# Optimization experiments

Measured on AMD Instinct MI355X. Metric: run time of the kernel, lower is better.

Reference implementation:

```python
import jax, jax.numpy as jnp
import numpy as np

N = 8192
IN_F = 256
HEADS = 4
HF = 64            # head_features = out_features / heads
OUT_F = HEADS * HF # concat=True
NEG_SLOPE = 0.2


def setup_inputs() -> dict:
    key = jax.random.key(0)
    ks = jax.random.split(key, 7)
    x = jax.random.normal(ks[0], (N, IN_F), dtype=jnp.float32)
    graph = jax.random.randint(ks[1], (N, N), 0, 2, dtype=jnp.int32)
    weight = jax.random.normal(ks[2], (HEADS, IN_F, HF), dtype=jnp.float32) * (1.0 / np.sqrt(IN_F))
    weight_i = jax.random.normal(ks[3], (HEADS, HF, 1), dtype=jnp.float32) * (1.0 / np.sqrt(HF))
    weight_j = jax.random.normal(ks[4], (HEADS, HF, 1), dtype=jnp.float32) * (1.0 / np.sqrt(HF))
    weight_r = jax.random.normal(ks[5], (IN_F, HF * HEADS), dtype=jnp.float32) * (1.0 / np.sqrt(IN_F))
    bias = jnp.zeros((OUT_F,), dtype=jnp.float32)
    return {"x": x, "graph": graph, "weight": weight, "weight_i": weight_i,
            "weight_j": weight_j, "weight_r": weight_r, "bias": bias}


def reference(x, graph, weight, weight_i, weight_j, weight_r, bias):
    # h: per-head projected features [heads, N, hf]
    h = jnp.einsum('nm,hmf->hnf', x, weight)
    # additive attention logits: coe_i [h,N,1] + coe_j [h,1,N]
    coe_i = jnp.einsum('hnf,hfo->hno', h, weight_i)          # [heads, N, 1]
    coe_j = jnp.einsum('hnf,hfo->hno', h, weight_j)          # [heads, N, 1]
    coe = jax.nn.leaky_relu(coe_i + jnp.swapaxes(coe_j, 1, 2), NEG_SLOPE)  # [heads, N, N]
    # adjacency mask (note transpose, matching the torch code)
    mask = jnp.where(graph > 0, 0.0, -jnp.inf).T             # [N, N]
    att = jax.nn.softmax(coe + mask[None], axis=-1)          # [heads, N, N]
    # aggregate and move heads to axis 1: [N, heads, hf]
    y = jnp.einsum('hij,hjf->ihf', att, h)
    # residual with projection (in_features != head_features)
    y = y + (x @ weight_r).reshape(N, HEADS, HF)
    # concat heads + bias
    y = y.reshape(N, OUT_F) + bias
    return y
```

## Files before the change

### kernel.cpp

```cpp
#include <hip/hip_runtime.h>
#include <hip/hip_bf16.h>

#define N 8192
#define IN_F 256
#define HEADS 4
#define HF 64
#define OUT_F 256

typedef __attribute__((ext_vector_type(8))) short short8;
typedef __attribute__((ext_vector_type(4))) float f32x4;

__device__ __forceinline__ float lrelu(float x) {
    return fmaxf(x, 0.0f) * 0.8f + x * 0.2f;
}
__device__ __forceinline__ short f2bf(float f) {
    union { __hip_bfloat16 h; short s; } u;
    u.h = __float2bfloat16(f);
    return u.s;
}
__device__ __forceinline__ float bf2f(unsigned short b) {
    union { unsigned u; float f; } v; v.u = ((unsigned)b) << 16;
    return v.f;
}

__global__ __launch_bounds__(256) void k_wcvt(
    const float* __restrict__ w, const float* __restrict__ wr,
    unsigned short* __restrict__ BbT)
{
    int c = blockIdx.x;
    int k = threadIdx.x;
    float v;
    if (c < 256) {
        int head = c >> 6, f = c & 63;
        v = w[((size_t)head * IN_F + k) * HF + f];
    } else {
        v = wr[(size_t)k * OUT_F + (c - 256)];
    }
    BbT[(size_t)c * IN_F + k] = (unsigned short)f2bf(v);
}

__global__ __launch_bounds__(256) void k_gemm(
    const float* __restrict__ x, const unsigned short* __restrict__ BbT,
    const float* __restrict__ bias,
    unsigned short* __restrict__ h, float* __restrict__ out)
{
    __shared__ unsigned short Asw[64 * 64];
    __shared__ unsigned short Bsw[128 * 64];
    int t = threadIdx.x;
    int m0 = blockIdx.x * 64;
    int bn = blockIdx.y;
    int w_ = t >> 6, l = t & 63;
    int wr_ = w_ >> 1, wc_ = w_ & 1;
    int ar = l & 15, g = l >> 4;

    f32x4 acc[2][4];
    #pragma unroll
    for (int m = 0; m < 2; ++m)
        #pragma unroll
        for (int n = 0; n < 4; ++n) acc[m][n] = (f32x4){0.f, 0.f, 0.f, 0.f};

    int srow = t >> 2, skq = (t & 3) * 16;
    int sc = t >> 1, sh = (t & 1) * 32;

    for (int kt = 0; kt < 4; ++kt) {
        const float* xs = x + (size_t)(m0 + srow) * IN_F + kt * 64 + skq;
        float4 xa = ((const float4*)xs)[0];
        float4 xb = ((const float4*)xs)[1];
        float4 xc = ((const float4*)xs)[2];
        float4 xd = ((const float4*)xs)[3];
        unsigned short ae[16];
        ae[0] = f2bf(xa.x); ae[1] = f2bf(xa.y); ae[2] = f2bf(xa.z); ae[3] = f2bf(xa.w);
        ae[4] = f2bf(xb.x); ae[5] = f2bf(xb.y); ae[6] = f2bf(xb.z); ae[7] = f2bf(xb.w);
        ae[8] = f2bf(xc.x); ae[9] = f2bf(xc.y); ae[10] = f2bf(xc.z); ae[11] = f2bf(xc.w);
        ae[12] = f2bf(xd.x); ae[13] = f2bf(xd.y); ae[14] = f2bf(xd.z); ae[15] = f2bf(xd.w);
        int kb0 = (skq >> 3) ^ (srow & 7);
        int kb1 = ((skq >> 3) + 1) ^ (srow & 7);
        *(uint4*)&Asw[srow * 64 + kb0 * 8] = *(uint4*)&ae[0];
        *(uint4*)&Asw[srow * 64 + kb1 * 8] = *(uint4*)&ae[8];
        const unsigned short* bs = BbT + (size_t)(bn * 128 + sc) * IN_F + kt * 64 + sh;
        uint4 b0 = ((const uint4*)bs)[0];
        uint4 b1 = ((const uint4*)bs)[1];
        uint4 b2 = ((const uint4*)bs)[2];
        uint4 b3 = ((const uint4*)bs)[3];
        int hb = sh >> 3;
        *(uint4*)&Bsw[sc * 64 + ((hb + 0) ^ (sc & 7)) * 8] = b0;
        *(uint4*)&Bsw[sc * 64 + ((hb + 1) ^ (sc & 7)) * 8] = b1;
        *(uint4*)&Bsw[sc * 64 + ((hb + 2) ^ (sc & 7)) * 8] = b2;
        *(uint4*)&Bsw[sc * 64 + ((hb + 3) ^ (sc & 7)) * 8] = b3;
        __syncthreads();
        #pragma unroll
        for (int ks = 0; ks < 2; ++ks) {
            short8 af[2], bf[4];
            #pragma unroll
            for (int m = 0; m < 2; ++m) {
                int row = wr_ * 32 + m * 16 + ar;
                int kb = (ks * 4 + g) ^ (row & 7);
                af[m] = *(const short8*)&Asw[row * 64 + kb * 8];
            }
            #pragma unroll
            for (int n = 0; n < 4; ++n) {
                int c = wc_ * 64 + n * 16 + ar;
                int kb = (ks * 4 + g) ^ (c & 7);
                bf[n] = *(const short8*)&Bsw[c * 64 + kb * 8];
            }
            #pragma unroll
            for (int m = 0; m < 2; ++m)
                #pragma unroll
                for (int n = 0; n < 4; ++n)
                    acc[m][n] = __builtin_amdgcn_mfma_f32_16x16x32_bf16(af[m], bf[n], acc[m][n], 0, 0, 0);
        }
        __syncthreads();
    }
    #pragma unroll
    for (int m = 0; m < 2; ++m) {
        #pragma unroll
        for (int n = 0; n < 4; ++n) {
            int cg = bn * 128 + wc_ * 64 + n * 16 + ar;
            #pragma unroll
            for (int r = 0; r < 4; ++r) {
                int mg = m0 + wr_ * 32 + m * 16 + g * 4 + r;
                float v = acc[m][n][r];
                if (cg < 256) {
                    int head = cg >> 6, f = cg & 63;
                    h[((size_t)head * N + mg) * HF + f] = (unsigned short)f2bf(v);
                } else {
                    out[(size_t)mg * OUT_F + (cg - 256)] = v + bias[cg - 256];
                }
            }
        }
    }
}

__global__ __launch_bounds__(256) void k_tr(
    const unsigned short* __restrict__ h, const float* __restrict__ wi,
    const float* __restrict__ wj,
    unsigned short* __restrict__ hT, float* __restrict__ coe_i, float* __restrict__ coe_j)
{
    __shared__ unsigned short tl[64 * 66];
    __shared__ float red_i[4][64];
    __shared__ float red_j[4][64];
    int t = threadIdx.x;
    int head = blockIdx.y;
    int n0 = blockIdx.x * 64;
    int nr = t >> 2, c0 = (t & 3) * 16;
    const unsigned short* src = h + ((size_t)(head * N + n0 + nr) * HF) + c0;
    uint4 v0 = *(const uint4*)src;
    uint4 v1 = *(const uint4*)(src + 8);
    unsigned short e[16];
    *(uint4*)&e[0] = v0;
    *(uint4*)&e[8] = v1;
    #pragma unroll
    for (int k = 0; k < 16; ++k)
        tl[(c0 + k) * 66 + nr] = e[k];
    __syncthreads();
    int f = t >> 2, nc = (t & 3) * 16;
    unsigned int ov[8];
    #pragma unroll
    for (int k = 0; k < 8; ++k)
        ov[k] = *(const unsigned int*)&tl[f * 66 + nc + 2 * k];
    unsigned short* dst = hT + ((size_t)(head * HF + f) * N) + n0 + nc;
    uint4 o0, o1;
    o0.x = ov[0]; o0.y = ov[1]; o0.z = ov[2]; o0.w = ov[3];
    o1.x = ov[4]; o1.y = ov[5]; o1.z = ov[6]; o1.w = ov[7];
    *(uint4*)dst = o0;
    *(uint4*)(dst + 8) = o1;
    int q = t >> 6, nn = t & 63;
    float pi = 0.f, pj = 0.f;
    #pragma unroll
    for (int k = 0; k < 16; ++k) {
        int ff = q * 16 + k;
        float hv = bf2f(tl[ff * 66 + nn]);
        pi = fmaf(hv, wi[head * HF + ff], pi);
        pj = fmaf(hv, wj[head * HF + ff], pj);
    }
    red_i[q][nn] = pi;
    red_j[q][nn] = pj;
    __syncthreads();
    if (t < 64) {
        float si = red_i[0][t] + red_i[1][t] + red_i[2][t] + red_i[3][t];
        float sj = red_j[0][t] + red_j[1][t] + red_j[2][t] + red_j[3][t];
        coe_i[head * N + n0 + t] = si;
        coe_j[head * N + n0 + t] = sj;
    }
}

__global__ __launch_bounds__(256) void k_cols(
    const float* __restrict__ coe_j, float* __restrict__ maxB,
    float* __restrict__ F, float* __restrict__ H)
{
    __shared__ float red[256];
    int head = blockIdx.x;
    int t = threadIdx.x;
    float m = -1e30f;
    for (int n = t; n < N; n += 256) {
        float b = coe_j[head * N + n];
        F[head * N + n] = __expf(b);
        H[head * N + n] = __expf(0.2f * b);
        m = fmaxf(m, b);
    }
    red[t] = m;
    __syncthreads();
    for (int s = 128; s > 0; s >>= 1) {
        if (t < s) red[t] = fmaxf(red[t], red[t + s]);
        __syncthreads();
    }
    if (t == 0) maxB[head] = red[0];
}

__global__ __launch_bounds__(256) void k_pack(
    const int* __restrict__ graph, unsigned int* __restrict__ bits)
{
    int i = blockIdx.y * 256 + threadIdx.x;
    int jw = blockIdx.x;
    const int* gp = graph + (size_t)(jw * 32) * N + i;
    unsigned int word = 0;
    #pragma unroll
    for (int k = 0; k < 32; ++k)
        word |= (gp[(size_t)k * N] > 0 ? 1u : 0u) << k;
    bits[(size_t)jw * N + i] = word;
}

__device__ __forceinline__ void computeP(short8& af,
    const float4& fa, const float4& fb, const float4& ha, const float4& hb,
    unsigned int mk, float Ei, float Gi)
{
    float fv[8] = {fa.x, fa.y, fa.z, fa.w, fb.x, fb.y, fb.z, fb.w};
    float hv[8] = {ha.x, ha.y, ha.z, ha.w, hb.x, hb.y, hb.z, hb.w};
    #pragma unroll
    for (int j = 0; j < 8; ++j) {
        float p = fmaxf(Ei * fv[j], Gi * hv[j]);
        p = (mk & (1u << j)) ? p : 0.0f;
        af[j] = f2bf(p);
    }
}

__global__ __launch_bounds__(512) void k_att(
    const unsigned short* __restrict__ hT, const float* __restrict__ coe_i,
    const float* __restrict__ maxB, const float* __restrict__ F,
    const float* __restrict__ H, const unsigned int* __restrict__ bits,
    float* __restrict__ out)
{
    __shared__ unsigned short hbuf[2][64 * 64];
    __shared__ float mbuf[4 * 64 * 21];

    int t = threadIdx.x;
    int head = blockIdx.x;
    int i0 = blockIdx.y * 64;
    int w = t >> 6;
    int l = t & 63;
    int wrow = w & 3;
    int grp = w >> 2;
    int ar = l & 15, g = l >> 4, g8 = g * 8;

    int irow = i0 + wrow * 16 + ar;
    float a = coe_i[head * N + irow];
    float M = lrelu(a + maxB[head]);
    float Ei = __expf(a - M);
    float Gi = __expf(0.2f * a - M);

    f32x4 acc[4];
    #pragma unroll
    for (int fb = 0; fb < 4; ++fb) acc[fb] = (f32x4){0.f, 0.f, 0.f, 0.f};
    f32x4 accd = (f32x4){0.f, 0.f, 0.f, 0.f};

    short8 ones;
    #pragma unroll
    for (int k = 0; k < 8; ++k) ones[k] = (short)0x3F80;

    int sbuf = t >> 8;
    int u = t & 255;
    int sf = u >> 2;
    int sj = (u & 3) * 16;
    const unsigned short* hrow = hT + ((size_t)(head * HF + sf) * N) + sj;
    int pg0 = ((sj >> 3) + 0) ^ (sf & 7);
    int pg1 = ((sj >> 3) + 1) ^ (sf & 7);
    unsigned short* wp0 = &hbuf[sbuf][sf * 64 + pg0 * 8];
    unsigned short* wp1 = &hbuf[sbuf][sf * 64 + pg1 * 8];

    const float* Fp = F + head * N + g8;
    const float* Hp = H + head * N + g8;
    const unsigned int* bp = bits + irow;

    for (int jt0 = 0; jt0 < N; jt0 += 128) {
        int jt = jt0 + grp * 64;
        uint4 hv0 = *(const uint4*)(hrow + jt0 + sbuf * 64);
        uint4 hv1 = *(const uint4*)(hrow + jt0 + sbuf * 64 + 8);
        unsigned int mk0 = bp[(size_t)((jt >> 5) + 0) * N] >> g8;
        unsigned int mk1 = bp[(size_t)((jt >> 5) + 1) * N] >> g8;
        float4 f0 = *(const float4*)(Fp + jt);
        float4 f1 = *(const float4*)(Fp + jt + 4);
        float4 f2 = *(const float4*)(Fp + jt + 32);
        float4 f3 = *(const float4*)(Fp + jt + 36);
        float4 h0 = *(const float4*)(Hp + jt);
        float4 h1 = *(const float4*)(Hp + jt + 4);
        float4 h2 = *(const float4*)(Hp + jt + 32);
        float4 h3 = *(const float4*)(Hp + jt + 36);

        __syncthreads();
        *(uint4*)wp0 = hv0;
        *(uint4*)wp1 = hv1;
        __syncthreads();

        short8 af0, af1;
        computeP(af0, f0, f1, h0, h1, mk0, Ei, Gi);
        computeP(af1, f2, f3, h2, h3, mk1, Ei, Gi);

        #pragma unroll
        for (int ss = 0; ss < 2; ++ss) {
            short8 af = ss ? af1 : af0;
            #pragma unroll
            for (int fb = 0; fb < 4; ++fb) {
                int row = fb * 16 + ar;
                int pg = (ss * 4 + g) ^ (ar & 7);
                short8 bfr = *(const short8*)&hbuf[grp][row * 64 + pg * 8];
                acc[fb] = __builtin_amdgcn_mfma_f32_16x16x32_bf16(af, bfr, acc[fb], 0, 0, 0);
            }
            accd = __builtin_amdgcn_mfma_f32_16x16x32_bf16(af, ones, accd, 0, 0, 0);
        }
    }

    __syncthreads();
    int mb = (wrow * 64 + l) * 21;
    if (grp == 1) {
        #pragma unroll
        for (int fb = 0; fb < 4; ++fb)
            #pragma unroll
            for (int r = 0; r < 4; ++r)
                mbuf[mb + fb * 4 + r] = acc[fb][r];
        #pragma unroll
        for (int r = 0; r < 4; ++r)
            mbuf[mb + 16 + r] = accd[r];
    }
    __syncthreads();
    if (grp == 0) {
        #pragma unroll
        for (int fb = 0; fb < 4; ++fb)
            #pragma unroll
            for (int r = 0; r < 4; ++r)
                acc[fb][r] += mbuf[mb + fb * 4 + r];
        #pragma unroll
        for (int r = 0; r < 4; ++r)
            accd[r] += mbuf[mb + 16 + r];
        #pragma unroll
        for (int r = 0; r < 4; ++r) {
            float inv = 1.0f / accd[r];
            int orow = i0 + wrow * 16 + g * 4 + r;
            float* op = out + (size_t)orow * OUT_F + head * HF + ar;
            #pragma unroll
            for (int fb = 0; fb < 4; ++fb)
                op[fb * 16] += acc[fb][r] * inv;
        }
    }
}

extern "C" void kernel_launch(void* const* d_in, const int* in_sizes, int n_in,
                              void* d_out, int out_size, void* d_ws, size_t ws_size,
                              hipStream_t stream) {
    const float* x     = (const float*)d_in[0];
    const int*   graph = (const int*)d_in[1];
    const float* w     = (const float*)d_in[2];
    const float* wi    = (const float*)d_in[3];
    const float* wj    = (const float*)d_in[4];
    const float* wr    = (const float*)d_in[5];
    const float* bias  = (const float*)d_in[6];
    float* out = (float*)d_out;

    char* ws = (char*)d_ws;
    unsigned short* h   = (unsigned short*)(ws);
    unsigned short* hT  = (unsigned short*)(ws + (4u << 20));
    float* coe_i = (float*)(ws + (8u << 20));
    float* coe_j = (float*)(ws + (8u << 20) + 131072);
    float* maxB  = (float*)(ws + (8u << 20) + 2 * 131072);
    float* F     = (float*)(ws + (8u << 20) + 2 * 131072 + 1024);
    float* H     = (float*)(ws + (8u << 20) + 3 * 131072 + 1024);
    unsigned short* BbT = (unsigned short*)(ws + (8u << 20) + 4 * 131072 + 1024);
    unsigned int* bits  = (unsigned int*)(ws + (8u << 20) + 4 * 131072 + 1024 + 262144);

    k_wcvt<<<dim3(512), 256, 0, stream>>>(w, wr, BbT);
    k_gemm<<<dim3(128, 4), 256, 0, stream>>>(x, BbT, bias, h, out);
    k_tr<<<dim3(128, 4), 256, 0, stream>>>(h, wi, wj, hT, coe_i, coe_j);
    k_cols<<<dim3(4), 256, 0, stream>>>(coe_j, maxB, F, H);
    k_pack<<<dim3(256, 32), 256, 0, stream>>>(graph, bits);
    k_att<<<dim3(HEADS, N / 64), 512, 0, stream>>>(hT, coe_i, maxB, F, H, bits, out);
}
```

Measured before the change: 180.9 us.

## Write transposed h from GEMM, register-prefetch attention tiles, pack bf16 conversions

The GEMM epilogue now writes h directly in transposed layout, so the separate transpose kernel is removed and replaced by a simple coefficient kernel that reads hT. The attention kernel prefetches the next hT tile into registers and double-buffers shared memory, which drops one barrier per iteration. It also aliases the merge buffer onto the same shared memory, swaps the grid axes, adds a launch-bounds occupancy hint, and builds P with packed bf16 conversion and branchless masking. The aim is to cut an intermediate round trip through memory and reduce barrier stalls in the main loop, at the cost of more register pressure and strided 8-byte stores from the GEMM.

```diff
diff --git a/kernel.cpp b/kernel.cpp
--- a/kernel.cpp
+++ b/kernel.cpp
@@ -21,6 +21,11 @@
 __device__ __forceinline__ float bf2f(unsigned short b) {
     union { unsigned u; float f; } v; v.u = ((unsigned)b) << 16;
     return v.f;
+}
+__device__ __forceinline__ unsigned pack_bf16(float p0, float p1) {
+    union { __hip_bfloat162 b; unsigned u; } cv;
+    cv.b = __float22bfloat162_rn(make_float2(p0, p1));
+    return cv.u;
 }
 
 __global__ __launch_bounds__(256) void k_wcvt(
@@ -42,7 +47,7 @@
 __global__ __launch_bounds__(256) void k_gemm(
     const float* __restrict__ x, const unsigned short* __restrict__ BbT,
     const float* __restrict__ bias,
-    unsigned short* __restrict__ h, float* __restrict__ out)
+    unsigned short* __restrict__ hT, float* __restrict__ out)
 {
     __shared__ unsigned short Asw[64 * 64];
     __shared__ unsigned short Bsw[128 * 64];
@@ -68,15 +73,15 @@
         float4 xb = ((const float4*)xs)[1];
         float4 xc = ((const float4*)xs)[2];
         float4 xd = ((const float4*)xs)[3];
-        unsigned short ae[16];
-        ae[0] = f2bf(xa.x); ae[1] = f2bf(xa.y); ae[2] = f2bf(xa.z); ae[3] = f2bf(xa.w);
-        ae[4] = f2bf(xb.x); ae[5] = f2bf(xb.y); ae[6] = f2bf(xb.z); ae[7] = f2bf(xb.w);
-        ae[8] = f2bf(xc.x); ae[9] = f2bf(xc.y); ae[10] = f2bf(xc.z); ae[11] = f2bf(xc.w);
-        ae[12] = f2bf(xd.x); ae[13] = f2bf(xd.y); ae[14] = f2bf(xd.z); ae[15] = f2bf(xd.w);
+        unsigned ae[8];
+        ae[0] = pack_bf16(xa.x, xa.y); ae[1] = pack_bf16(xa.z, xa.w);
+        ae[2] = pack_bf16(xb.x, xb.y); ae[3] = pack_bf16(xb.z, xb.w);
+        ae[4] = pack_bf16(xc.x, xc.y); ae[5] = pack_bf16(xc.z, xc.w);
+        ae[6] = pack_bf16(xd.x, xd.y); ae[7] = pack_bf16(xd.z, xd.w);
         int kb0 = (skq >> 3) ^ (srow & 7);
         int kb1 = ((skq >> 3) + 1) ^ (srow & 7);
         *(uint4*)&Asw[srow * 64 + kb0 * 8] = *(uint4*)&ae[0];
-        *(uint4*)&Asw[srow * 64 + kb1 * 8] = *(uint4*)&ae[8];
+        *(uint4*)&Asw[srow * 64 + kb1 * 8] = *(uint4*)&ae[4];
         const unsigned short* bs = BbT + (size_t)(bn * 128 + sc) * IN_F + kt * 64 + sh;
         uint4 b0 = ((const uint4*)bs)[0];
         uint4 b1 = ((const uint4*)bs)[1];
@@ -116,72 +121,39 @@
         #pragma unroll
         for (int n = 0; n < 4; ++n) {
             int cg = bn * 128 + wc_ * 64 + n * 16 + ar;
-            #pragma unroll
-            for (int r = 0; r < 4; ++r) {
-                int mg = m0 + wr_ * 32 + m * 16 + g * 4 + r;
-                float v = acc[m][n][r];
-                if (cg < 256) {
-                    int head = cg >> 6, f = cg & 63;
-                    h[((size_t)head * N + mg) * HF + f] = (unsigned short)f2bf(v);
-                } else {
-                    out[(size_t)mg * OUT_F + (cg - 256)] = v + bias[cg - 256];
-                }
+            int mg0 = m0 + wr_ * 32 + m * 16 + g * 4;
+            if (cg < 256) {
+                int head = cg >> 6, f = cg & 63;
+                unsigned pk[2];
+                pk[0] = pack_bf16(acc[m][n][0], acc[m][n][1]);
+                pk[1] = pack_bf16(acc[m][n][2], acc[m][n][3]);
+                *(uint2*)(hT + (size_t)(head * HF + f) * N + mg0) = *(uint2*)pk;
+            } else {
+                float bb = bias[cg - 256];
+                #pragma unroll
+                for (int r = 0; r < 4; ++r)
+                    out[(size_t)(mg0 + r) * OUT_F + (cg - 256)] = acc[m][n][r] + bb;
             }
         }
     }
 }
 
-__global__ __launch_bounds__(256) void k_tr(
-    const unsigned short* __restrict__ h, const float* __restrict__ wi,
-    const float* __restrict__ wj,
-    unsigned short* __restrict__ hT, float* __restrict__ coe_i, float* __restrict__ coe_j)
-{
-    __shared__ unsigned short tl[64 * 66];
-    __shared__ float red_i[4][64];
-    __shared__ float red_j[4][64];
-    int t = threadIdx.x;
+__global__ __launch_bounds__(256) void k_coe(
+    const unsigned short* __restrict__ hT, const float* __restrict__ wi,
+    const float* __restrict__ wj, float* __restrict__ coe_i, float* __restrict__ coe_j)
+{
     int head = blockIdx.y;
-    int n0 = blockIdx.x * 64;
-    int nr = t >> 2, c0 = (t & 3) * 16;
-    const unsigned short* src = h + ((size_t)(head * N + n0 + nr) * HF) + c0;
-    uint4 v0 = *(const uint4*)src;
-    uint4 v1 = *(const uint4*)(src + 8);
-    unsigned short e[16];
-    *(uint4*)&e[0] = v0;
-    *(uint4*)&e[8] = v1;
-    #pragma unroll
-    for (int k = 0; k < 16; ++k)
-        tl[(c0 + k) * 66 + nr] = e[k];
-    __syncthreads();
-    int f = t >> 2, nc = (t & 3) * 16;
-    unsigned int ov[8];
-    #pragma unroll
-    for (int k = 0; k < 8; ++k)
-        ov[k] = *(const unsigned int*)&tl[f * 66 + nc + 2 * k];
-    unsigned short* dst = hT + ((size_t)(head * HF + f) * N) + n0 + nc;
-    uint4 o0, o1;
-    o0.x = ov[0]; o0.y = ov[1]; o0.z = ov[2]; o0.w = ov[3];
-    o1.x = ov[4]; o1.y = ov[5]; o1.z = ov[6]; o1.w = ov[7];
-    *(uint4*)dst = o0;
-    *(uint4*)(dst + 8) = o1;
-    int q = t >> 6, nn = t & 63;
-    float pi = 0.f, pj = 0.f;
-    #pragma unroll
-    for (int k = 0; k < 16; ++k) {
-        int ff = q * 16 + k;
-        float hv = bf2f(tl[ff * 66 + nn]);
-        pi = fmaf(hv, wi[head * HF + ff], pi);
-        pj = fmaf(hv, wj[head * HF + ff], pj);
-    }
-    red_i[q][nn] = pi;
-    red_j[q][nn] = pj;
-    __syncthreads();
-    if (t < 64) {
-        float si = red_i[0][t] + red_i[1][t] + red_i[2][t] + red_i[3][t];
-        float sj = red_j[0][t] + red_j[1][t] + red_j[2][t] + red_j[3][t];
-        coe_i[head * N + n0 + t] = si;
-        coe_j[head * N + n0 + t] = sj;
-    }
+    int n = blockIdx.x * 256 + threadIdx.x;
+    const unsigned short* hp = hT + (size_t)head * HF * N + n;
+    float si = 0.f, sj = 0.f;
+    #pragma unroll 8
+    for (int f = 0; f < HF; ++f) {
+        float hv = bf2f(hp[(size_t)f * N]);
+        si = fmaf(hv, wi[head * HF + f], si);
+        sj = fmaf(hv, wj[head * HF + f], sj);
+    }
+    coe_i[head * N + n] = si;
+    coe_j[head * N + n] = sj;
 }
 
 __global__ __launch_bounds__(256) void k_cols(
@@ -220,36 +192,41 @@
     bits[(size_t)jw * N + i] = word;
 }
 
-__device__ __forceinline__ void computeP(short8& af,
-    const float4& fa, const float4& fb, const float4& ha, const float4& hb,
+__device__ __forceinline__ short8 makeP(
+    const float4& fa, const float4& fb2, const float4& ha, const float4& hb2,
     unsigned int mk, float Ei, float Gi)
 {
-    float fv[8] = {fa.x, fa.y, fa.z, fa.w, fb.x, fb.y, fb.z, fb.w};
-    float hv[8] = {ha.x, ha.y, ha.z, ha.w, hb.x, hb.y, hb.z, hb.w};
-    #pragma unroll
-    for (int j = 0; j < 8; ++j) {
-        float p = fmaxf(Ei * fv[j], Gi * hv[j]);
-        p = (mk & (1u << j)) ? p : 0.0f;
-        af[j] = f2bf(p);
-    }
-}
-
-__global__ __launch_bounds__(512) void k_att(
+    float fv[8] = {fa.x, fa.y, fa.z, fa.w, fb2.x, fb2.y, fb2.z, fb2.w};
+    float hv[8] = {ha.x, ha.y, ha.z, ha.w, hb2.x, hb2.y, hb2.z, hb2.w};
+    union { short8 s8; unsigned u[4]; } A;
+    #pragma unroll
+    for (int jp = 0; jp < 4; ++jp) {
+        float p0 = fmaxf(Ei * fv[2 * jp],     Gi * hv[2 * jp]);
+        float p1 = fmaxf(Ei * fv[2 * jp + 1], Gi * hv[2 * jp + 1]);
+        int s0 = ((int)(mk << (31 - 2 * jp))) >> 31;
+        int s1 = ((int)(mk << (30 - 2 * jp))) >> 31;
+        p0 = __int_as_float(__float_as_int(p0) & s0);
+        p1 = __int_as_float(__float_as_int(p1) & s1);
+        A.u[jp] = pack_bf16(p0, p1);
+    }
+    return A.s8;
+}
+
+__global__ __launch_bounds__(512, 8) void k_att(
     const unsigned short* __restrict__ hT, const float* __restrict__ coe_i,
     const float* __restrict__ maxB, const float* __restrict__ F,
     const float* __restrict__ H, const unsigned int* __restrict__ bits,
     float* __restrict__ out)
 {
-    __shared__ unsigned short hbuf[2][64 * 64];
-    __shared__ float mbuf[4 * 64 * 21];
+    __shared__ char smem[32768];
+    unsigned short* hb = (unsigned short*)smem;
+    float* mbuf = (float*)smem;
 
     int t = threadIdx.x;
-    int head = blockIdx.x;
-    int i0 = blockIdx.y * 64;
-    int w = t >> 6;
-    int l = t & 63;
-    int wrow = w & 3;
-    int grp = w >> 2;
+    int head = blockIdx.y;
+    int i0 = blockIdx.x * 64;
+    int w = t >> 6, l = t & 63;
+    int wrow = w & 3, grp = w >> 2;
     int ar = l & 15, g = l >> 4, g8 = g * 8;
 
     int irow = i0 + wrow * 16 + ar;
@@ -269,24 +246,24 @@
 
     int sbuf = t >> 8;
     int u = t & 255;
-    int sf = u >> 2;
-    int sj = (u & 3) * 16;
+    int sf = u >> 2, sj = (u & 3) * 16;
     const unsigned short* hrow = hT + ((size_t)(head * HF + sf) * N) + sj;
     int pg0 = ((sj >> 3) + 0) ^ (sf & 7);
     int pg1 = ((sj >> 3) + 1) ^ (sf & 7);
-    unsigned short* wp0 = &hbuf[sbuf][sf * 64 + pg0 * 8];
-    unsigned short* wp1 = &hbuf[sbuf][sf * 64 + pg1 * 8];
+    int wo = sbuf * 4096 + sf * 64;
 
     const float* Fp = F + head * N + g8;
     const float* Hp = H + head * N + g8;
     const unsigned int* bp = bits + irow;
 
-    for (int jt0 = 0; jt0 < N; jt0 += 128) {
-        int jt = jt0 + grp * 64;
-        uint4 hv0 = *(const uint4*)(hrow + jt0 + sbuf * 64);
-        uint4 hv1 = *(const uint4*)(hrow + jt0 + sbuf * 64 + 8);
-        unsigned int mk0 = bp[(size_t)((jt >> 5) + 0) * N] >> g8;
-        unsigned int mk1 = bp[(size_t)((jt >> 5) + 1) * N] >> g8;
+    uint4 hv0 = *(const uint4*)(hrow + sbuf * 64);
+    uint4 hv1 = *(const uint4*)(hrow + sbuf * 64 + 8);
+
+    for (int s = 0; s < 64; ++s) {
+        int jt = s * 128 + grp * 64;
+        size_t jw = (size_t)(jt >> 5);
+        unsigned int mk0 = bp[jw * N] >> g8;
+        unsigned int mk1 = bp[(jw + 1) * N] >> g8;
         float4 f0 = *(const float4*)(Fp + jt);
         float4 f1 = *(const float4*)(Fp + jt + 4);
         float4 f2 = *(const float4*)(Fp + jt + 32);
@@ -295,16 +272,18 @@
         float4 h1 = *(const float4*)(Hp + jt + 4);
         float4 h2 = *(const float4*)(Hp + jt + 32);
         float4 h3 = *(const float4*)(Hp + jt + 36);
-
+        int bo = (s & 1) * 8192;
+        *(uint4*)&hb[bo + wo + pg0 * 8] = hv0;
+        *(uint4*)&hb[bo + wo + pg1 * 8] = hv1;
+        int sn = (s + 1 < 64) ? s + 1 : s;
+        hv0 = *(const uint4*)(hrow + sn * 128 + sbuf * 64);
+        hv1 = *(const uint4*)(hrow + sn * 128 + sbuf * 64 + 8);
         __syncthreads();
-        *(uint4*)wp0 = hv0;
-        *(uint4*)wp1 = hv1;
-        __syncthreads();
-
-        short8 af0, af1;
-        computeP(af0, f0, f1, h0, h1, mk0, Ei, Gi);
-        computeP(af1, f2, f3, h2, h3, mk1, Ei, Gi);
-
+
+        short8 af0 = makeP(f0, f1, h0, h1, mk0, Ei, Gi);
+        short8 af1 = makeP(f2, f3, h2, h3, mk1, Ei, Gi);
+
+        const unsigned short* rb = &hb[bo + grp * 4096];
         #pragma unroll
         for (int ss = 0; ss < 2; ++ss) {
             short8 af = ss ? af1 : af0;
@@ -312,7 +291,7 @@
             for (int fb = 0; fb < 4; ++fb) {
                 int row = fb * 16 + ar;
                 int pg = (ss * 4 + g) ^ (ar & 7);
-                short8 bfr = *(const short8*)&hbuf[grp][row * 64 + pg * 8];
+                short8 bfr = *(const short8*)&rb[row * 64 + pg * 8];
                 acc[fb] = __builtin_amdgcn_mfma_f32_16x16x32_bf16(af, bfr, acc[fb], 0, 0, 0);
             }
             accd = __builtin_amdgcn_mfma_f32_16x16x32_bf16(af, ones, accd, 0, 0, 0);
@@ -366,20 +345,19 @@
     float* out = (float*)d_out;
 
     char* ws = (char*)d_ws;
-    unsigned short* h   = (unsigned short*)(ws);
-    unsigned short* hT  = (unsigned short*)(ws + (4u << 20));
-    float* coe_i = (float*)(ws + (8u << 20));
-    float* coe_j = (float*)(ws + (8u << 20) + 131072);
-    float* maxB  = (float*)(ws + (8u << 20) + 2 * 131072);
-    float* F     = (float*)(ws + (8u << 20) + 2 * 131072 + 1024);
-    float* H     = (float*)(ws + (8u << 20) + 3 * 131072 + 1024);
-    unsigned short* BbT = (unsigned short*)(ws + (8u << 20) + 4 * 131072 + 1024);
-    unsigned int* bits  = (unsigned int*)(ws + (8u << 20) + 4 * 131072 + 1024 + 262144);
+    unsigned short* hT  = (unsigned short*)(ws);
+    float* coe_i = (float*)(ws + 4194304);
+    float* coe_j = (float*)(ws + 4325376);
+    float* maxB  = (float*)(ws + 4456448);
+    float* F     = (float*)(ws + 4457472);
+    float* H     = (float*)(ws + 4588544);
+    unsigned short* BbT = (unsigned short*)(ws + 4719616);
+    unsigned int* bits  = (unsigned int*)(ws + 4981760);
 
     k_wcvt<<<dim3(512), 256, 0, stream>>>(w, wr, BbT);
-    k_gemm<<<dim3(128, 4), 256, 0, stream>>>(x, BbT, bias, h, out);
-    k_tr<<<dim3(128, 4), 256, 0, stream>>>(h, wi, wj, hT, coe_i, coe_j);
+    k_gemm<<<dim3(128, 4), 256, 0, stream>>>(x, BbT, bias, hT, out);
+    k_coe<<<dim3(32, 4), 256, 0, stream>>>(hT, wi, wj, coe_i, coe_j);
     k_cols<<<dim3(4), 256, 0, stream>>>(coe_j, maxB, F, H);
     k_pack<<<dim3(256, 32), 256, 0, stream>>>(graph, bits);
-    k_att<<<dim3(HEADS, N / 64), 512, 0, stream>>>(hT, coe_i, maxB, F, H, bits, out);
-}
+    k_att<<<dim3(N / 64, HEADS), 512, 0, stream>>>(hT, coe_i, maxB, F, H, bits, out);
+}
```

Result: slower. 254.4 us (+40.7%).
